# Performance work log

Hardware: AMD Instinct MI355X
Metric: run time of the kernel (lower is better)

## Reference

```python
import jax, jax.numpy as jnp
import numpy as np

S, B, H, NH = 2048, 1, 4096, 32
HD = H // NH            # 128
ROT = int(HD * 0.25)    # 32 partial rotary dims
BASE = 10000.0


def setup_inputs() -> dict:
    key = jax.random.key(0)
    ks = jax.random.split(key, 4)
    hidden_states = jax.random.normal(ks[0], (S, B, H), dtype=jnp.float32)
    W_qkv = jax.random.normal(ks[1], (3 * H, H), dtype=jnp.float32) * 0.02
    b_qkv = jnp.zeros((3 * H,), dtype=jnp.float32)
    W_dense = jax.random.normal(ks[2], (H, H), dtype=jnp.float32) * 0.02
    b_dense = jnp.zeros((H,), dtype=jnp.float32)
    # causal left-to-right mask, True = attend
    attention_mask = jnp.tril(jnp.ones((S, S), dtype=bool))[None, None]  # [1,1,S,S]
    return dict(hidden_states=hidden_states, attention_mask=attention_mask,
                W_qkv=W_qkv, b_qkv=b_qkv, W_dense=W_dense, b_dense=b_dense)


def _rotate_half(x):
    x1, x2 = jnp.split(x, 2, axis=-1)
    return jnp.concatenate((-x2, x1), axis=-1)


def reference(hidden_states, attention_mask, W_qkv, b_qkv, W_dense, b_dense):
    S_, B_ = hidden_states.shape[:2]
    qkv = hidden_states @ W_qkv.T + b_qkv                    # [S,B,3H]
    qkv = qkv.reshape(S_, B_, NH, 3 * HD)
    q, k, v = qkv[..., :HD], qkv[..., HD:2 * HD], qkv[..., 2 * HD:]

    # partial rotary embedding (GPT-NeoX style, offset=0, no KV cache)
    inv_freq = 1.0 / (BASE ** (jnp.arange(0, ROT, 2, dtype=jnp.float32) / ROT))
    t = jnp.arange(S_, dtype=jnp.float32)
    freqs = jnp.einsum('s,d->sd', t, inv_freq)               # [S,ROT/2]
    emb = jnp.concatenate((freqs, freqs), axis=-1)           # [S,ROT]
    cos = jnp.cos(emb)[:, None, None, :]                     # [S,1,1,ROT]
    sin = jnp.sin(emb)[:, None, None, :]

    def rope(x):
        return x * cos + _rotate_half(x) * sin

    q = jnp.concatenate((rope(q[..., :ROT]), q[..., ROT:]), axis=-1)
    k = jnp.concatenate((rope(k[..., :ROT]), k[..., ROT:]), axis=-1)

    # scaled dot-product attention with explicit score matrix
    scores = jnp.einsum('sbhd,tbhd->bhst', q, k) / np.float32(np.sqrt(HD))
    scores = jnp.where(attention_mask, scores, jnp.float32(-10000.0))
    probs = jax.nn.softmax(scores, axis=-1)                  # [B,NH,S,S]
    ctx = jnp.einsum('bhst,tbhd->sbhd', probs, v).reshape(S_, B_, H)
    return ctx @ W_dense.T + b_dense                         # [S,B,H]
```

## Files before the change

kernel.cpp:

```cpp
#include <hip/hip_runtime.h>
#include <hip/hip_bf16.h>
#include <math.h>

typedef __bf16 bf16_t;
typedef bf16_t bf16x8 __attribute__((ext_vector_type(8)));
typedef bf16_t bf16x4 __attribute__((ext_vector_type(4)));
typedef float floatx4 __attribute__((ext_vector_type(4)));

#define S_LEN 2048
#define QK_LD 8192

__global__ void convert_all(const float* __restrict__ a, bf16_t* __restrict__ ao,
                            const float* __restrict__ b, bf16_t* __restrict__ bo,
                            const float* __restrict__ c, bf16_t* __restrict__ co) {
    int i = blockIdx.x * 256 + threadIdx.x;
    const float* src; bf16_t* dst; int j;
    if (i < 2097152)        { src = a; dst = ao; j = i; }
    else if (i < 14680064)  { src = b; dst = bo; j = i - 2097152; }
    else                    { src = c; dst = co; j = i - 14680064; }
    float4 v = ((const float4*)src)[j];
    bf16x4 o;
    o.x = (bf16_t)v.x; o.y = (bf16_t)v.y; o.z = (bf16_t)v.z; o.w = (bf16_t)v.w;
    ((bf16x4*)dst)[j] = o;
}

__device__ __forceinline__ void async_copy16(const void* g, void* l) {
    __builtin_amdgcn_global_load_lds(
        (const __attribute__((address_space(1))) unsigned int*)g,
        (__attribute__((address_space(3))) unsigned int*)l, 16, 0, 0);
}

__device__ __forceinline__ void fast_sincos(float x, float* sn, float* cs) {
    float rev = x * 0.15915494309189535f;
    rev = rev - floorf(rev);
    *sn = __builtin_amdgcn_sinf(rev);
    *cs = __builtin_amdgcn_cosf(rev);
}

__global__ __launch_bounds__(512, 2) void qkv_gemm256(
    const bf16_t* __restrict__ A, const bf16_t* __restrict__ B,
    const float* __restrict__ bias, bf16_t* __restrict__ qkout,
    bf16_t* __restrict__ vt)
{
    __shared__ bf16_t lds[65536];
    const int t = threadIdx.x;
    const int lane = t & 63;
    const int w = t >> 6;
    const int l15 = lane & 15, quad = lane >> 4;
    const int wr = w >> 2, wc = w & 3;
    const int x = blockIdx.x & 7;
    const int j = blockIdx.x >> 3;
    const int bm = j / 6;
    const int bn = x * 6 + (j % 6);

    const int srow = t >> 2;
    const int kslot8 = ((t & 3) ^ ((t >> 3) & 3)) << 3;
    const bf16_t* Ag = A + (size_t)(bm * 256 + srow) * 4096 + kslot8;
    const bf16_t* Bg = B + (size_t)(bn * 256 + srow) * 4096 + kslot8;
    bf16_t* ldsW = lds + t * 8;

    const int xorv8 = (quad ^ ((l15 >> 1) & 3)) << 3;
    const bf16_t* pA0 = lds + (wr * 128 + l15) * 32 + xorv8;
    const bf16_t* pB0 = lds + 32768 + (wc * 64 + l15) * 32 + xorv8;

    floatx4 acc[8][4];
    #pragma unroll
    for (int i = 0; i < 8; i++)
        #pragma unroll
        for (int jj = 0; jj < 4; jj++)
            acc[i][jj] = (floatx4){0.f, 0.f, 0.f, 0.f};

    bf16x8 a[4], b[4];

#define STAGE_A(tile, kh, dd) do { \
    const bf16_t* g_ = Ag + (tile) * 64 + (kh) * 32; \
    bf16_t* l_ = ldsW + ((dd) * 2 + (kh)) * 8192; \
    async_copy16(g_, l_); \
    async_copy16(g_ + (size_t)128 * 4096, l_ + 4096); \
} while (0)
#define STAGE_B(tile, kh, dd) do { \
    const bf16_t* g_ = Bg + (tile) * 64 + (kh) * 32; \
    bf16_t* l_ = ldsW + 32768 + ((dd) * 2 + (kh)) * 8192; \
    async_copy16(g_, l_); \
    async_copy16(g_ + (size_t)128 * 4096, l_ + 4096); \
} while (0)
#define LOAD_B4(dd, kh) do { \
    const bf16_t* pb_ = pB0 + ((dd) * 2 + (kh)) * 8192; \
    b[0] = *(const bf16x8*)(pb_ + 0 * 512); \
    b[1] = *(const bf16x8*)(pb_ + 1 * 512); \
    b[2] = *(const bf16x8*)(pb_ + 2 * 512); \
    b[3] = *(const bf16x8*)(pb_ + 3 * 512); \
} while (0)
#define LOAD_A4(dd, kh, ph) do { \
    const bf16_t* pa_ = pA0 + ((dd) * 2 + (kh)) * 8192 + (ph) * 2048; \
    a[0] = *(const bf16x8*)(pa_ + 0 * 512); \
    a[1] = *(const bf16x8*)(pa_ + 1 * 512); \
    a[2] = *(const bf16x8*)(pa_ + 2 * 512); \
    a[3] = *(const bf16x8*)(pa_ + 3 * 512); \
} while (0)
#define MFMA16(ph) do { \
    __builtin_amdgcn_s_setprio(1); \
    _Pragma("unroll") \
    for (int mi_ = 0; mi_ < 4; mi_++) \
        _Pragma("unroll") \
        for (int ni_ = 0; ni_ < 4; ni_++) \
            acc[(ph) * 4 + mi_][ni_] = __builtin_amdgcn_mfma_f32_16x16x32_bf16( \
                a[mi_], b[ni_], acc[(ph) * 4 + mi_][ni_], 0, 0, 0); \
    __builtin_amdgcn_s_setprio(0); \
} while (0)
#define PH_MID() do { \
    __builtin_amdgcn_sched_barrier(0); \
    __builtin_amdgcn_s_barrier(); \
    asm volatile("s_waitcnt lgkmcnt(0)" ::: "memory"); \
    __builtin_amdgcn_sched_barrier(0); \
} while (0)
#define PH_END() do { \
    __builtin_amdgcn_sched_barrier(0); \
    asm volatile("" ::: "memory"); \
    __builtin_amdgcn_s_barrier(); \
} while (0)

    STAGE_A(0, 0, 0); STAGE_B(0, 0, 0);
    STAGE_A(0, 1, 0); STAGE_B(0, 1, 0);
    STAGE_A(1, 0, 1); STAGE_B(1, 0, 1);
    asm volatile("s_waitcnt vmcnt(8)" ::: "memory");
    __builtin_amdgcn_s_barrier();

    for (int tt = 0; tt < 64; tt += 2) {
        LOAD_B4(0, 0); LOAD_A4(0, 0, 0);
        STAGE_A(tt + 1, 1, 1);
        PH_MID(); MFMA16(0); PH_END();

        LOAD_A4(0, 0, 1);
        STAGE_B(tt + 1, 1, 1);
        PH_MID(); MFMA16(1);
        asm volatile("s_waitcnt vmcnt(8)" ::: "memory");
        PH_END();

        LOAD_B4(0, 1); LOAD_A4(0, 1, 0);
        if (tt + 2 < 64) STAGE_A(tt + 2, 0, 0);
        PH_MID(); MFMA16(0); PH_END();

        LOAD_A4(0, 1, 1);
        if (tt + 2 < 64) STAGE_B(tt + 2, 0, 0);
        PH_MID(); MFMA16(1);
        if (tt + 2 < 64) { asm volatile("s_waitcnt vmcnt(8)" ::: "memory"); }
        else             { asm volatile("s_waitcnt vmcnt(4)" ::: "memory"); }
        PH_END();

        LOAD_B4(1, 0); LOAD_A4(1, 0, 0);
        if (tt + 2 < 64) STAGE_A(tt + 2, 1, 0);
        PH_MID(); MFMA16(0); PH_END();

        LOAD_A4(1, 0, 1);
        if (tt + 2 < 64) STAGE_B(tt + 2, 1, 0);
        PH_MID(); MFMA16(1);
        if (tt + 2 < 64) { asm volatile("s_waitcnt vmcnt(8)" ::: "memory"); }
        else             { asm volatile("s_waitcnt vmcnt(0)" ::: "memory"); }
        PH_END();

        LOAD_B4(1, 1); LOAD_A4(1, 1, 0);
        if (tt + 3 < 64) STAGE_A(tt + 3, 0, 1);
        PH_MID(); MFMA16(0); PH_END();

        LOAD_A4(1, 1, 1);
        if (tt + 3 < 64) STAGE_B(tt + 3, 0, 1);
        PH_MID(); MFMA16(1);
        if (tt + 3 < 64) { asm volatile("s_waitcnt vmcnt(8)" ::: "memory"); }
        PH_END();
    }

#undef STAGE_A
#undef STAGE_B
#undef LOAD_B4
#undef LOAD_A4
#undef MFMA16
#undef PH_MID
#undef PH_END

    const int colbase = bn * 256 + wc * 64;
    #pragma unroll
    for (int ni = 0; ni < 4; ni++) {
        const int cb = colbase + ni * 16;
        const float bv = bias[cb + l15];
        const int h = cb / 384;
        const int rem = cb - h * 384;
        if (rem < 256) {
            bf16_t* qb = qkout + (size_t)h * 256 + rem + l15;
            #pragma unroll
            for (int mi = 0; mi < 8; mi++) {
                const int row0 = bm * 256 + wr * 128 + mi * 16 + quad * 4;
                #pragma unroll
                for (int r = 0; r < 4; r++)
                    qb[(size_t)(row0 + r) * QK_LD] = (bf16_t)(acc[mi][ni][r] + bv);
            }
        } else {
            const int d0 = rem - 256 + l15;
            bf16_t* vb = vt + ((size_t)h * 128 + d0) * S_LEN;
            #pragma unroll
            for (int mi = 0; mi < 8; mi++) {
                const int row0 = bm * 256 + wr * 128 + mi * 16 + quad * 4;
                bf16x4 pv;
                #pragma unroll
                for (int r = 0; r < 4; r++) pv[r] = (bf16_t)(acc[mi][ni][r] + bv);
                *(bf16x4*)&vb[row0] = pv;
            }
        }
    }
}

__global__ void rope_kernel(bf16_t* __restrict__ qk) {
    int idx = blockIdx.x * 256 + threadIdx.x;
    int j = idx & 15;
    int h = (idx >> 4) & 31;
    int s = idx >> 9;
    float invf = exp2f(-(float)j * 0.8304820237218405f);
    float sn, cs;
    fast_sincos((float)s * invf, &sn, &cs);
    bf16_t* base = qk + (size_t)s * QK_LD + h * 256;
    {
        float x1 = (float)base[j], x2 = (float)base[j + 16];
        base[j]      = (bf16_t)(x1 * cs - x2 * sn);
        base[j + 16] = (bf16_t)(x2 * cs + x1 * sn);
    }
    {
        bf16_t* kb = base + 128;
        float x1 = (float)kb[j], x2 = (float)kb[j + 16];
        kb[j]      = (bf16_t)(x1 * cs - x2 * sn);
        kb[j + 16] = (bf16_t)(x2 * cs + x1 * sn);
    }
}

__global__ __launch_bounds__(256) void dense_gemm128(
    const bf16_t* __restrict__ A, const bf16_t* __restrict__ B,
    const float* __restrict__ bias, float* __restrict__ C)
{
    const int K = 4096, N = 4096;
    __shared__ bf16_t As[128 * 32];
    __shared__ bf16_t Bs[128 * 32];
    const int t    = threadIdx.x;
    const int lane = t & 63;
    const int w    = t >> 6;
    const int l15  = lane & 15;
    const int quad = lane >> 4;
    const int x = blockIdx.x & 7;
    const int j = blockIdx.x >> 3;
    const int bn = x * 4 + (j & 3);
    const int bm = j >> 2;
    const int mw = (w >> 1) * 64, nw = (w & 1) * 64;

    floatx4 acc[4][4];
    #pragma unroll
    for (int i = 0; i < 4; i++)
        #pragma unroll
        for (int jj = 0; jj < 4; jj++)
            acc[i][jj] = (floatx4){0.f, 0.f, 0.f, 0.f};

    const int r0 = t >> 2;
    const int c0 = (t & 3) * 8;
    const bf16_t* Aptr = A + (size_t)(bm * 128 + r0) * K + c0;
    const bf16_t* Bptr = B + (size_t)(bn * 128 + r0) * K + c0;
    bf16_t* AsW = As + t * 8;
    bf16_t* BsW = Bs + t * 8;

    for (int k0 = 0; k0 < K; k0 += 32) {
        __syncthreads();
        async_copy16(Aptr + k0, AsW);
        async_copy16(Aptr + k0 + (size_t)64 * K, AsW + 2048);
        async_copy16(Bptr + k0, BsW);
        async_copy16(Bptr + k0 + (size_t)64 * K, BsW + 2048);
        __syncthreads();

        bf16x8 a[4], b[4];
        #pragma unroll
        for (int mi = 0; mi < 4; mi++)
            a[mi] = *(const bf16x8*)&As[(mw + mi * 16 + l15) * 32 + quad * 8];
        #pragma unroll
        for (int ni = 0; ni < 4; ni++)
            b[ni] = *(const bf16x8*)&Bs[(nw + ni * 16 + l15) * 32 + quad * 8];
        #pragma unroll
        for (int mi = 0; mi < 4; mi++)
            #pragma unroll
            for (int ni = 0; ni < 4; ni++)
                acc[mi][ni] = __builtin_amdgcn_mfma_f32_16x16x32_bf16(a[mi], b[ni], acc[mi][ni], 0, 0, 0);
    }

    #pragma unroll
    for (int ni = 0; ni < 4; ni++) {
        int col = bn * 128 + nw + ni * 16 + l15;
        float bv = bias[col];
        #pragma unroll
        for (int mi = 0; mi < 4; mi++)
            #pragma unroll
            for (int r = 0; r < 4; r++) {
                int row = bm * 128 + mw + mi * 16 + quad * 4 + r;
                C[(size_t)row * N + col] = acc[mi][ni][r] + bv;
            }
    }
}

#define QK_LDS 136
#define V_LDS  72
__global__ __launch_bounds__(256) void flash_attn(
    const bf16_t* __restrict__ qk, const bf16_t* __restrict__ Vt,
    bf16_t* __restrict__ ctx)
{
    __shared__ bf16_t Qs[64 * QK_LDS];
    __shared__ bf16_t Ks[64 * QK_LDS];
    __shared__ bf16_t Vs[128 * V_LDS];
    __shared__ bf16_t Ps[64 * V_LDS];
    const int h = blockIdx.y;
    const int qb = (int)gridDim.x - 1 - blockIdx.x;
    const int t = threadIdx.x;
    const int w = t >> 6, lane = t & 63;
    const int quad = lane >> 4, l15 = lane & 15;
    const float SCL = 0.08838834764831845f * 1.4426950408889634f;

    const int rr = t >> 4, cc = (t & 15) * 8;
    const int vr = t >> 3, vc = (t & 7) * 8;

    {
        const bf16_t* qbase = qk + (size_t)(qb * 64) * QK_LD + h * 256;
        #pragma unroll
        for (int p = 0; p < 4; p++) {
            int row = rr + p * 16;
            *(bf16x8*)&Qs[row * QK_LDS + cc] = *(const bf16x8*)&qbase[(size_t)row * QK_LD + cc];
        }
    }

    bf16x8 kreg[4], vreg[4];
#define LOAD_KV(kt_) do { \
    const bf16_t* kb_ = qk + (size_t)((kt_) * 64) * QK_LD + h * 256 + 128; \
    _Pragma("unroll") \
    for (int p = 0; p < 4; p++) \
        kreg[p] = *(const bf16x8*)&kb_[(size_t)(rr + p * 16) * QK_LD + cc]; \
    const bf16_t* vb_ = Vt + (size_t)h * 128 * S_LEN + (kt_) * 64; \
    _Pragma("unroll") \
    for (int p = 0; p < 4; p++) \
        vreg[p] = *(const bf16x8*)&vb_[(size_t)(vr + p * 32) * S_LEN + vc]; \
} while (0)

    floatx4 o[8];
    #pragma unroll
    for (int i = 0; i < 8; i++) o[i] = (floatx4){0.f, 0.f, 0.f, 0.f};
    float lsum[4] = {0.f, 0.f, 0.f, 0.f};

    LOAD_KV(0);

    for (int kt = 0; kt <= qb; kt++) {
        __syncthreads();
        #pragma unroll
        for (int p = 0; p < 4; p++)
            *(bf16x8*)&Ks[(rr + p * 16) * QK_LDS + cc] = kreg[p];
        #pragma unroll
        for (int p = 0; p < 4; p++)
            *(bf16x8*)&Vs[(vr + p * 32) * V_LDS + vc] = vreg[p];
        __syncthreads();
        if (kt < qb) LOAD_KV(kt + 1);

        floatx4 sacc[4];
        #pragma unroll
        for (int ni = 0; ni < 4; ni++) sacc[ni] = (floatx4){0.f, 0.f, 0.f, 0.f};
        __builtin_amdgcn_s_setprio(1);
        #pragma unroll
        for (int ks = 0; ks < 4; ks++) {
            bf16x8 aq = *(const bf16x8*)&Qs[(w * 16 + l15) * QK_LDS + ks * 32 + quad * 8];
            #pragma unroll
            for (int ni = 0; ni < 4; ni++) {
                bf16x8 bk = *(const bf16x8*)&Ks[(ni * 16 + l15) * QK_LDS + ks * 32 + quad * 8];
                sacc[ni] = __builtin_amdgcn_mfma_f32_16x16x32_bf16(aq, bk, sacc[ni], 0, 0, 0);
            }
        }
        __builtin_amdgcn_s_setprio(0);

        float pv[4][4];
        #pragma unroll
        for (int ni = 0; ni < 4; ni++)
            #pragma unroll
            for (int r = 0; r < 4; r++)
                pv[ni][r] = __builtin_amdgcn_exp2f(sacc[ni][r] * SCL);
        if (kt == qb) {
            #pragma unroll
            for (int ni = 0; ni < 4; ni++) {
                int key = ni * 16 + l15;
                #pragma unroll
                for (int r = 0; r < 4; r++)
                    if (key > w * 16 + quad * 4 + r) pv[ni][r] = 0.f;
            }
        }
        #pragma unroll
        for (int ni = 0; ni < 4; ni++)
            #pragma unroll
            for (int r = 0; r < 4; r++) {
                lsum[r] += pv[ni][r];
                Ps[(w * 16 + quad * 4 + r) * V_LDS + ni * 16 + l15] = (bf16_t)pv[ni][r];
            }
        asm volatile("s_waitcnt lgkmcnt(0)" ::: "memory");

        __builtin_amdgcn_s_setprio(1);
        #pragma unroll
        for (int ks = 0; ks < 2; ks++) {
            bf16x8 ap = *(const bf16x8*)&Ps[(w * 16 + l15) * V_LDS + ks * 32 + quad * 8];
            #pragma unroll
            for (int ni = 0; ni < 8; ni++) {
                bf16x8 bv = *(const bf16x8*)&Vs[(ni * 16 + l15) * V_LDS + ks * 32 + quad * 8];
                o[ni] = __builtin_amdgcn_mfma_f32_16x16x32_bf16(ap, bv, o[ni], 0, 0, 0);
            }
        }
        __builtin_amdgcn_s_setprio(0);
    }
#undef LOAD_KV

    float invl[4];
    #pragma unroll
    for (int r = 0; r < 4; r++) {
        float s = lsum[r];
        #pragma unroll
        for (int off = 1; off < 16; off <<= 1)
            s += __shfl_xor(s, off, 16);
        invl[r] = 1.f / s;
    }
    bf16_t* cbase = ctx + (size_t)(qb * 64) * 4096 + h * 128;
    #pragma unroll
    for (int ni = 0; ni < 8; ni++) {
        int col = ni * 16 + l15;
        #pragma unroll
        for (int r = 0; r < 4; r++) {
            int row = w * 16 + quad * 4 + r;
            cbase[(size_t)row * 4096 + col] = (bf16_t)(o[ni][r] * invl[r]);
        }
    }
}

extern "C" void kernel_launch(void* const* d_in, const int* in_sizes, int n_in,
                              void* d_out, int out_size, void* d_ws, size_t ws_size,
                              hipStream_t stream) {
    const float* hidden = (const float*)d_in[0];
    const float* Wqkv   = (const float*)d_in[2];
    const float* bqkv   = (const float*)d_in[3];
    const float* Wd     = (const float*)d_in[4];
    const float* bd     = (const float*)d_in[5];
    float* out = (float*)d_out;

    char* ws = (char*)d_ws;
    bf16_t* h_bf    = (bf16_t*)(ws);
    bf16_t* wqkv_bf = (bf16_t*)(ws + 16777216);
    bf16_t* wd_bf   = (bf16_t*)(ws + 117440512);
    bf16_t* qk      = (bf16_t*)(ws + 150994944);
    bf16_t* vt      = (bf16_t*)(ws + 184549376);
    bf16_t* ctx     = (bf16_t*)(ws + 201326592);

    convert_all<<<73728, 256, 0, stream>>>(hidden, h_bf, Wqkv, wqkv_bf, Wd, wd_bf);
    qkv_gemm256<<<dim3(384), 512, 0, stream>>>(h_bf, wqkv_bf, bqkv, qk, vt);
    rope_kernel<<<4096, 256, 0, stream>>>(qk);
    flash_attn<<<dim3(32, 32), 256, 0, stream>>>(qk, vt, ctx);
    dense_gemm128<<<dim3(512), 256, 0, stream>>>(ctx, wd_bf, bd, out);
}
```

Measured before the change: 794.3 us.

## Fuse partial rotary embedding into QKV GEMM epilogue and keep Q in registers

Applies the partial RoPE rotation directly in the QKV GEMM epilogue for the first 32 dims of Q and K column blocks, which removes the separate rope kernel launch and its read-modify-write pass over Q/K. The flash attention kernel now loads the Q fragments straight from global memory into registers instead of staging them through shared memory. This frees LDS and drops per-iteration LDS reads of Q, at the cost of more live registers and extra sincos work in the GEMM epilogue.

```diff
diff --git a/kernel.cpp b/kernel.cpp
--- a/kernel.cpp
+++ b/kernel.cpp
@@ -179,23 +179,49 @@
 #undef PH_END
 
     const int colbase = bn * 256 + wc * 64;
-    #pragma unroll
-    for (int ni = 0; ni < 4; ni++) {
-        const int cb = colbase + ni * 16;
-        const float bv = bias[cb + l15];
-        const int h = cb / 384;
-        const int rem = cb - h * 384;
-        if (rem < 256) {
-            bf16_t* qb = qkout + (size_t)h * 256 + rem + l15;
+    const int h = colbase / 384;
+    const int rem0 = colbase - h * 384;
+    if (rem0 < 256) {
+        bf16_t* qb = qkout + (size_t)h * 256 + rem0 + l15;
+        float bv[4];
+        #pragma unroll
+        for (int ni = 0; ni < 4; ni++) bv[ni] = bias[colbase + ni * 16 + l15];
+        if (rem0 == 0 || rem0 == 128) {
+            const float invf = exp2f(-(float)l15 * 0.8304820237218405f);
             #pragma unroll
             for (int mi = 0; mi < 8; mi++) {
                 const int row0 = bm * 256 + wr * 128 + mi * 16 + quad * 4;
                 #pragma unroll
-                for (int r = 0; r < 4; r++)
-                    qb[(size_t)(row0 + r) * QK_LD] = (bf16_t)(acc[mi][ni][r] + bv);
+                for (int r = 0; r < 4; r++) {
+                    const int row = row0 + r;
+                    float sn, cs;
+                    fast_sincos((float)row * invf, &sn, &cs);
+                    const float x1 = acc[mi][0][r] + bv[0];
+                    const float x2 = acc[mi][1][r] + bv[1];
+                    qb[(size_t)row * QK_LD]      = (bf16_t)(x1 * cs - x2 * sn);
+                    qb[(size_t)row * QK_LD + 16] = (bf16_t)(x2 * cs + x1 * sn);
+                    qb[(size_t)row * QK_LD + 32] = (bf16_t)(acc[mi][2][r] + bv[2]);
+                    qb[(size_t)row * QK_LD + 48] = (bf16_t)(acc[mi][3][r] + bv[3]);
+                }
             }
         } else {
-            const int d0 = rem - 256 + l15;
+            #pragma unroll
+            for (int mi = 0; mi < 8; mi++) {
+                const int row0 = bm * 256 + wr * 128 + mi * 16 + quad * 4;
+                #pragma unroll
+                for (int r = 0; r < 4; r++) {
+                    const int row = row0 + r;
+                    #pragma unroll
+                    for (int ni = 0; ni < 4; ni++)
+                        qb[(size_t)row * QK_LD + ni * 16] = (bf16_t)(acc[mi][ni][r] + bv[ni]);
+                }
+            }
+        }
+    } else {
+        #pragma unroll
+        for (int ni = 0; ni < 4; ni++) {
+            const float bv = bias[colbase + ni * 16 + l15];
+            const int d0 = rem0 + ni * 16 - 256 + l15;
             bf16_t* vb = vt + ((size_t)h * 128 + d0) * S_LEN;
             #pragma unroll
             for (int mi = 0; mi < 8; mi++) {
@@ -206,28 +232,6 @@
                 *(bf16x4*)&vb[row0] = pv;
             }
         }
-    }
-}
-
-__global__ void rope_kernel(bf16_t* __restrict__ qk) {
-    int idx = blockIdx.x * 256 + threadIdx.x;
-    int j = idx & 15;
-    int h = (idx >> 4) & 31;
-    int s = idx >> 9;
-    float invf = exp2f(-(float)j * 0.8304820237218405f);
-    float sn, cs;
-    fast_sincos((float)s * invf, &sn, &cs);
-    bf16_t* base = qk + (size_t)s * QK_LD + h * 256;
-    {
-        float x1 = (float)base[j], x2 = (float)base[j + 16];
-        base[j]      = (bf16_t)(x1 * cs - x2 * sn);
-        base[j + 16] = (bf16_t)(x2 * cs + x1 * sn);
-    }
-    {
-        bf16_t* kb = base + 128;
-        float x1 = (float)kb[j], x2 = (float)kb[j + 16];
-        kb[j]      = (bf16_t)(x1 * cs - x2 * sn);
-        kb[j + 16] = (bf16_t)(x2 * cs + x1 * sn);
     }
 }
 
@@ -305,7 +309,6 @@
     const bf16_t* __restrict__ qk, const bf16_t* __restrict__ Vt,
     bf16_t* __restrict__ ctx)
 {
-    __shared__ bf16_t Qs[64 * QK_LDS];
     __shared__ bf16_t Ks[64 * QK_LDS];
     __shared__ bf16_t Vs[128 * V_LDS];
     __shared__ bf16_t Ps[64 * V_LDS];
@@ -319,13 +322,12 @@
     const int rr = t >> 4, cc = (t & 15) * 8;
     const int vr = t >> 3, vc = (t & 7) * 8;
 
+    bf16x8 qreg[4];
     {
-        const bf16_t* qbase = qk + (size_t)(qb * 64) * QK_LD + h * 256;
-        #pragma unroll
-        for (int p = 0; p < 4; p++) {
-            int row = rr + p * 16;
-            *(bf16x8*)&Qs[row * QK_LDS + cc] = *(const bf16x8*)&qbase[(size_t)row * QK_LD + cc];
-        }
+        const bf16_t* qrow = qk + (size_t)(qb * 64 + w * 16 + l15) * QK_LD + h * 256;
+        #pragma unroll
+        for (int ks = 0; ks < 4; ks++)
+            qreg[ks] = *(const bf16x8*)&qrow[ks * 32 + quad * 8];
     }
 
     bf16x8 kreg[4], vreg[4];
@@ -364,11 +366,10 @@
         __builtin_amdgcn_s_setprio(1);
         #pragma unroll
         for (int ks = 0; ks < 4; ks++) {
-            bf16x8 aq = *(const bf16x8*)&Qs[(w * 16 + l15) * QK_LDS + ks * 32 + quad * 8];
             #pragma unroll
             for (int ni = 0; ni < 4; ni++) {
                 bf16x8 bk = *(const bf16x8*)&Ks[(ni * 16 + l15) * QK_LDS + ks * 32 + quad * 8];
-                sacc[ni] = __builtin_amdgcn_mfma_f32_16x16x32_bf16(aq, bk, sacc[ni], 0, 0, 0);
+                sacc[ni] = __builtin_amdgcn_mfma_f32_16x16x32_bf16(qreg[ks], bk, sacc[ni], 0, 0, 0);
             }
         }
         __builtin_amdgcn_s_setprio(0);
@@ -452,7 +453,6 @@
 
     convert_all<<<73728, 256, 0, stream>>>(hidden, h_bf, Wqkv, wqkv_bf, Wd, wd_bf);
     qkv_gemm256<<<dim3(384), 512, 0, stream>>>(h_bf, wqkv_bf, bqkv, qk, vt);
-    rope_kernel<<<4096, 256, 0, stream>>>(qk);
     flash_attn<<<dim3(32, 32), 256, 0, stream>>>(qk, vt, ctx);
     dense_gemm128<<<dim3(512), 256, 0, stream>>>(ctx, wd_bf, bd, out);
 }
```

Measured after the change: 773.7 us. 1.03x faster.
